# Performance work log

Measured on AMD Instinct MI355X. Metric: run time of the kernel, lower is better.

## Reference

```python
import jax, jax.numpy as jnp
import numpy as np

N_NODES = 100000
N_EDGES = 1600000
N_GRAPHS = 2000
N_FEAT = 13


def gcn_conv(x, edge_index, W, b, n):
    """PyG GCNConv: h = D^{-1/2}(A+I)D^{-1/2} X W + b (add_self_loops, symmetric norm)."""
    h = x @ W  # [n, out]
    loop = jnp.arange(n, dtype=edge_index.dtype)
    src = jnp.concatenate([edge_index[0], loop])  # message sources (x_j)
    dst = jnp.concatenate([edge_index[1], loop])  # aggregation targets
    deg = jax.ops.segment_sum(jnp.ones_like(dst, dtype=h.dtype), dst, num_segments=n)
    dinv = jnp.where(deg > 0, jax.lax.rsqrt(jnp.maximum(deg, 1e-12)), 0.0)
    norm = dinv[src] * dinv[dst]  # [E+n]
    out = jax.ops.segment_sum(h[src] * norm[:, None], dst, num_segments=n)
    return out + b


def setup_inputs() -> dict:
    key = jax.random.key(0)
    ks = jax.random.split(key, 12)
    d = {}
    d["x"] = jax.random.normal(ks[0], (N_NODES, N_FEAT), dtype=jnp.float32)
    d["edge_index"] = jax.random.randint(ks[1], (2, N_EDGES), 0, N_NODES, dtype=jnp.int32)
    d["batch"] = jnp.sort(jax.random.randint(ks[2], (N_NODES,), 0, N_GRAPHS, dtype=jnp.int32))
    def lin(k, i, o):
        return jax.random.normal(k, (i, o), dtype=jnp.float32) * (1.0 / np.sqrt(i))
    d["W0"] = lin(ks[3], N_FEAT, 128); d["b0"] = jnp.zeros((128,), jnp.float32)
    d["W1"] = lin(ks[4], 128, 128);    d["b1"] = jnp.zeros((128,), jnp.float32)
    d["W2"] = lin(ks[5], 128, 128);    d["b2"] = jnp.zeros((128,), jnp.float32)
    d["Wf0"] = lin(ks[6], 128, 256);   d["bf0"] = jnp.zeros((256,), jnp.float32)
    d["Wf1"] = lin(ks[7], 256, 128);   d["bf1"] = jnp.zeros((128,), jnp.float32)
    d["Wo"] = lin(ks[8], 128, 1);      d["bo"] = jnp.zeros((1,), jnp.float32)
    return d


def reference(x, edge_index, batch, W0, b0, W1, b1, W2, b2, Wf0, bf0, Wf1, bf1, Wo, bo):
    n = x.shape[0]
    h = jax.nn.relu(gcn_conv(x, edge_index, W0, b0, n))
    h = jax.nn.relu(gcn_conv(h, edge_index, W1, b1, n))
    h = gcn_conv(h, edge_index, W2, b2, n)  # no relu after last conv
    # global mean pool over graphs
    cnt = jax.ops.segment_sum(jnp.ones((n,), h.dtype), batch, num_segments=N_GRAPHS)
    pooled = jax.ops.segment_sum(h, batch, num_segments=N_GRAPHS) / jnp.maximum(cnt, 1.0)[:, None]
    h = jax.nn.relu(pooled @ Wf0 + bf0)
    h = jax.nn.relu(h @ Wf1 + bf1)
    return h @ Wo + bo  # [N_GRAPHS, 1]
```

## Files before the change

kernel.cpp:

```cpp
#include <hip/hip_runtime.h>
#include <hip/hip_bf16.h>

#define N_NODES  100000
#define N_EDGES  1600000
#define N_GRAPHS 2000
#define N_FEAT   13
#define HID      128
#define NB       ((N_NODES + 127) / 128)
#define NBLK     128
#define N2       (NB * NBLK)

typedef __attribute__((ext_vector_type(8))) short bf16x8;
typedef __attribute__((ext_vector_type(4))) float f32x4;
typedef __attribute__((ext_vector_type(8))) unsigned short ushort8;

__global__ void k_hist1(const int* __restrict__ dst, int* __restrict__ counts, int E) {
    __shared__ int hist[NB];
    int k = blockIdx.x, t = threadIdx.x;
    for (int b = t; b < NB; b += 256) hist[b] = 0;
    __syncthreads();
    int epb = (E + NBLK - 1) / NBLK;
    int base = k * epb, lim = min(base + epb, E);
    for (int i = base + t; i < lim; i += 256) atomicAdd(&hist[dst[i] >> 7], 1);
    __syncthreads();
    for (int b = t; b < NB; b += 256) counts[k * NB + b] = hist[b];
}

__global__ void k_transp(const int* __restrict__ counts, int* __restrict__ countsT) {
    int i = blockIdx.x * 256 + threadIdx.x;
    if (i < N2) countsT[i] = counts[(i & (NBLK - 1)) * NB + (i >> 7)];
}

__global__ void k_scatter(const int* __restrict__ src, const int* __restrict__ dst,
                          const int* __restrict__ scT, unsigned int* __restrict__ bstore, int E) {
    __shared__ int cnt[NB];
    int k = blockIdx.x, t = threadIdx.x;
    for (int b = t; b < NB; b += 256) cnt[b] = 0;
    __syncthreads();
    int epb = (E + NBLK - 1) / NBLK;
    int base = k * epb, lim = min(base + epb, E);
    for (int i = base + t; i < lim; i += 256) {
        int d = dst[i];
        int b = d >> 7;
        int r = atomicAdd(&cnt[b], 1);
        bstore[scT[b * NBLK + k] + r] = ((unsigned int)src[i] << 7) | (unsigned int)(d & 127);
    }
}

__global__ void k_bhistx(const unsigned int* __restrict__ bstore, const int* __restrict__ scT,
                         const float* __restrict__ x, int* __restrict__ indeg,
                         float* __restrict__ dinv, float* __restrict__ xs, int n, int E) {
    __shared__ int cnt[128];
    int b = blockIdx.x, t = threadIdx.x;
    if (t < 128) cnt[t] = 0;
    __syncthreads();
    int start = scT[b * NBLK];
    int end = (b + 1 < NB) ? scT[(b + 1) * NBLK] : E;
    for (int i = start + t; i < end; i += 256) atomicAdd(&cnt[bstore[i] & 127], 1);
    __syncthreads();
    int node = b * 128 + t;
    if (t < 128 && node < n) {
        int c = cnt[t];
        indeg[node] = c;
        float dv = rsqrtf((float)(c + 1));
        dinv[node] = dv;
        float r[16];
#pragma unroll
        for (int k = 0; k < N_FEAT; k++) r[k] = dv * x[node * N_FEAT + k];
        r[13] = r[14] = r[15] = 0.f;
        float4* o = (float4*)&xs[(size_t)node * 16];
        o[0] = float4{r[0], r[1], r[2], r[3]};
        o[1] = float4{r[4], r[5], r[6], r[7]};
        o[2] = float4{r[8], r[9], r[10], r[11]};
        o[3] = float4{r[12], r[13], r[14], r[15]};
    }
}

__global__ void k_bfill(const unsigned int* __restrict__ bstore, const int* __restrict__ scT,
                        const int* __restrict__ off, int* __restrict__ csr, int n, int E) {
    __shared__ int cur[128];
    __shared__ int loff[128];
    int b = blockIdx.x, t = threadIdx.x;
    if (t < 128) {
        cur[t] = 0;
        int node = b * 128 + t;
        loff[t] = (node < n) ? off[node] : 0;
    }
    __syncthreads();
    int start = scT[b * NBLK];
    int end = (b + 1 < NB) ? scT[(b + 1) * NBLK] : E;
    for (int i = start + t; i < end; i += 256) {
        unsigned int e = bstore[i];
        int dl = e & 127;
        int p = loff[dl] + atomicAdd(&cur[dl], 1);
        csr[p] = (int)(e >> 7);
    }
}

__global__ void k_scan1(const int* __restrict__ in, int* __restrict__ out,
                        int* __restrict__ bsum, int n) {
    __shared__ int ts[256];
    int t = threadIdx.x;
    int base = blockIdx.x * 1024 + t * 4;
    int v0 = (base + 0 < n) ? in[base + 0] : 0;
    int v1 = (base + 1 < n) ? in[base + 1] : 0;
    int v2 = (base + 2 < n) ? in[base + 2] : 0;
    int v3 = (base + 3 < n) ? in[base + 3] : 0;
    int s = v0 + v1 + v2 + v3;
    ts[t] = s;
    __syncthreads();
    for (int o = 1; o < 256; o <<= 1) {
        int x = (t >= o) ? ts[t - o] : 0;
        __syncthreads();
        ts[t] += x;
        __syncthreads();
    }
    if (t == 255) bsum[blockIdx.x] = ts[255];
    int run = ts[t] - s;
    if (base + 0 < n) out[base + 0] = run; run += v0;
    if (base + 1 < n) out[base + 1] = run; run += v1;
    if (base + 2 < n) out[base + 2] = run; run += v2;
    if (base + 3 < n) out[base + 3] = run;
}

__global__ void k_scan_block(const int* __restrict__ in, int* __restrict__ out, int len) {
    __shared__ int ts[256];
    int t = threadIdx.x;
    int v[8];
    int s = 0;
#pragma unroll
    for (int j = 0; j < 8; j++) {
        int i = t * 8 + j;
        v[j] = (i < len) ? in[i] : 0;
        s += v[j];
    }
    ts[t] = s;
    __syncthreads();
    for (int o = 1; o < 256; o <<= 1) {
        int x = (t >= o) ? ts[t - o] : 0;
        __syncthreads();
        ts[t] += x;
        __syncthreads();
    }
    int run = ts[t] - s;
#pragma unroll
    for (int j = 0; j < 8; j++) {
        int i = t * 8 + j;
        if (i < len) out[i] = run;
        run += v[j];
    }
}

__global__ void k_scan3(int* __restrict__ out, const int* __restrict__ bpre, int n) {
    int i = blockIdx.x * 256 + threadIdx.x;
    if (i < n) out[i] += bpre[i >> 10];
}

__device__ __forceinline__ unsigned short f2bf(float f) {
    unsigned int b = __float_as_uint(f);
    b += 0x7fffu + ((b >> 16) & 1u);
    return (unsigned short)(b >> 16);
}

__device__ __forceinline__ void addrow8(float (&a)[8], uint4 v) {
    a[0] += __uint_as_float(v.x << 16);
    a[1] += __uint_as_float(v.x & 0xffff0000u);
    a[2] += __uint_as_float(v.y << 16);
    a[3] += __uint_as_float(v.y & 0xffff0000u);
    a[4] += __uint_as_float(v.z << 16);
    a[5] += __uint_as_float(v.z & 0xffff0000u);
    a[6] += __uint_as_float(v.w << 16);
    a[7] += __uint_as_float(v.w & 0xffff0000u);
}

__global__ __launch_bounds__(256) void k_gf13(const float* __restrict__ xs,
                                              const int* __restrict__ off,
                                              const int* __restrict__ indeg,
                                              const int* __restrict__ csr,
                                              const float* __restrict__ dinv,
                                              const float* __restrict__ W,
                                              const float* __restrict__ b,
                                              unsigned short* __restrict__ h, int n) {
    __shared__ float Ws[N_FEAT * HID];
    __shared__ __align__(16) float aggs[64][16];
    __shared__ float bs[HID];
    int t = threadIdx.x;
    for (int i = t; i < N_FEAT * HID; i += 256) Ws[i] = W[i];
    if (t < HID) bs[t] = b[t];
    int lane = t & 63;
    int slot = (t >> 6) * 16 + (lane >> 2);
    int l2 = lane & 3;
    int nb = blockIdx.x * 64;
    int d = nb + slot;
    const float4* X4 = (const float4*)xs;
    if (d < n) {
        int s0 = off[d], c = indeg[d];
        float4 acc = X4[(size_t)d * 4 + l2];
        int p = 0;
        for (; p + 7 < c; p += 8) {
            int s_[8];
#pragma unroll
            for (int j = 0; j < 8; j++) s_[j] = csr[s0 + p + j];
            float4 v[8];
#pragma unroll
            for (int j = 0; j < 8; j++) v[j] = X4[(size_t)s_[j] * 4 + l2];
#pragma unroll
            for (int j = 0; j < 8; j++) {
                acc.x += v[j].x; acc.y += v[j].y; acc.z += v[j].z; acc.w += v[j].w;
            }
        }
        for (; p < c; p++) {
            float4 v = X4[(size_t)csr[s0 + p] * 4 + l2];
            acc.x += v.x; acc.y += v.y; acc.z += v.z; acc.w += v.w;
        }
        float dv = dinv[d];
        float4 r = {dv * acc.x, dv * acc.y, dv * acc.z, dv * acc.w};
        *(float4*)&aggs[slot][l2 * 4] = r;
    }
    __syncthreads();
    int f = t & 127;
    int g0 = t >> 7;
    float wreg[N_FEAT];
#pragma unroll
    for (int k = 0; k < N_FEAT; k++) wreg[k] = Ws[k * HID + f];
#pragma unroll
    for (int j = 0; j < 32; j++) {
        int nl = g0 + j * 2;
        int dd = nb + nl;
        if (dd < n) {
            float acc = bs[f];
#pragma unroll
            for (int k = 0; k < N_FEAT; k++) acc += aggs[nl][k] * wreg[k];
            h[(size_t)dd * HID + f] = f2bf(fmaxf(acc, 0.f));
        }
    }
}

__global__ void k_wcast2(const float* __restrict__ W1, const float* __restrict__ W2,
                         unsigned short* __restrict__ Wt1, unsigned short* __restrict__ Wt2) {
    int i = blockIdx.x * 256 + threadIdx.x;
    if (i < HID * HID) {
        int c = i >> 7, k = i & 127;
        Wt1[i] = f2bf(W1[k * HID + c]);
        Wt2[i] = f2bf(W2[k * HID + c]);
    }
}

__global__ __launch_bounds__(256) void k_mfma128(const unsigned short* __restrict__ X,
                                                 const unsigned short* __restrict__ Wt,
                                                 const float* __restrict__ dinv,
                                                 unsigned short* __restrict__ ubf, int n) {
    int t = threadIdx.x;
    int wave = t >> 6, lane = t & 63;
    int lrow = lane & 15;
    int lk8 = (lane >> 4) * 8;
    int tile0 = blockIdx.x * 16 + wave * 4;

    f32x4 acc[4][8];
#pragma unroll
    for (int nt = 0; nt < 4; nt++)
#pragma unroll
        for (int ct = 0; ct < 8; ct++) acc[nt][ct] = f32x4{0.f, 0.f, 0.f, 0.f};

#pragma unroll
    for (int s = 0; s < 4; s++) {
        bf16x8 bfr[8];
#pragma unroll
        for (int ct = 0; ct < 8; ct++) {
            int col = ct * 16 + lrow;
            bfr[ct] = *(const bf16x8*)&Wt[col * HID + s * 32 + lk8];
        }
#pragma unroll
        for (int nt = 0; nt < 4; nt++) {
            int row = min((tile0 + nt) * 16 + lrow, n - 1);
            bf16x8 afr = *(const bf16x8*)&X[(size_t)row * HID + s * 32 + lk8];
#pragma unroll
            for (int ct = 0; ct < 8; ct++)
                acc[nt][ct] = __builtin_amdgcn_mfma_f32_16x16x32_bf16(afr, bfr[ct], acc[nt][ct], 0, 0, 0);
        }
    }

#pragma unroll
    for (int nt = 0; nt < 4; nt++) {
        int rbase = (tile0 + nt) * 16 + (lane >> 4) * 4;
#pragma unroll
        for (int r = 0; r < 4; r++) {
            int row = rbase + r;
            if (row < n) {
                float dv = dinv[row];
#pragma unroll
                for (int ct = 0; ct < 8; ct++)
                    ubf[(size_t)row * HID + ct * 16 + lrow] = f2bf(dv * acc[nt][ct][r]);
            }
        }
    }
}

__global__ void k_gather128(const unsigned int* __restrict__ ubf, const int* __restrict__ off,
                            const int* __restrict__ indeg, const int* __restrict__ csr,
                            const float* __restrict__ dinv, const float* __restrict__ bias,
                            unsigned short* __restrict__ yh, int n) {
    int t = threadIdx.x;
    int lane = t & 63;
    int quad = lane >> 4, l4 = lane & 15;
    int d = blockIdx.x * 16 + (t >> 6) * 4 + quad;
    if (d >= n) return;
    int s0 = off[d], c = indeg[d];
    const uint4* U = (const uint4*)ubf;

    uint4 sv = U[(size_t)d * 16 + l4];
    float a[8] = {0.f, 0.f, 0.f, 0.f, 0.f, 0.f, 0.f, 0.f};
    addrow8(a, sv);

    int p = 0;
    for (; p + 7 < c; p += 8) {
        int s_[8];
#pragma unroll
        for (int j = 0; j < 8; j++) s_[j] = csr[s0 + p + j];
        uint4 v[8];
#pragma unroll
        for (int j = 0; j < 8; j++) v[j] = U[(size_t)s_[j] * 16 + l4];
#pragma unroll
        for (int j = 0; j < 8; j++) addrow8(a, v[j]);
    }
    if (p + 3 < c) {
        int s_[4];
#pragma unroll
        for (int j = 0; j < 4; j++) s_[j] = csr[s0 + p + j];
        uint4 v[4];
#pragma unroll
        for (int j = 0; j < 4; j++) v[j] = U[(size_t)s_[j] * 16 + l4];
#pragma unroll
        for (int j = 0; j < 4; j++) addrow8(a, v[j]);
        p += 4;
    }
    for (; p < c; p++) addrow8(a, U[(size_t)csr[s0 + p] * 16 + l4]);

    float dv = dinv[d];
    float4 bb0 = *(const float4*)&bias[l4 * 8];
    float4 bb1 = *(const float4*)&bias[l4 * 8 + 4];
    float r[8];
    r[0] = dv * a[0] + bb0.x; r[1] = dv * a[1] + bb0.y;
    r[2] = dv * a[2] + bb0.z; r[3] = dv * a[3] + bb0.w;
    r[4] = dv * a[4] + bb1.x; r[5] = dv * a[5] + bb1.y;
    r[6] = dv * a[6] + bb1.z; r[7] = dv * a[7] + bb1.w;
    ushort8 hh;
#pragma unroll
    for (int j = 0; j < 8; j++) hh[j] = f2bf(fmaxf(r[j], 0.f));
    *(ushort8*)&yh[(size_t)d * HID + l4 * 8] = hh;
}

__global__ void k_gather128p(const unsigned int* __restrict__ ubf, const int* __restrict__ off,
                             const int* __restrict__ indeg, const int* __restrict__ csr,
                             const float* __restrict__ dinv, const float* __restrict__ bias,
                             const int* __restrict__ batch, float* __restrict__ pooledm, int n) {
    __shared__ __align__(16) float part[16][128];
    __shared__ int bid[16];
    int t = threadIdx.x;
    int lane = t & 63;
    int quad = lane >> 4, l4 = lane & 15;
    int slot = (t >> 6) * 4 + quad;
    int d = blockIdx.x * 16 + slot;
    const uint4* U = (const uint4*)ubf;
    if (d < n) {
        int s0 = off[d], c = indeg[d];
        uint4 sv = U[(size_t)d * 16 + l4];
        float a[8] = {0.f, 0.f, 0.f, 0.f, 0.f, 0.f, 0.f, 0.f};
        addrow8(a, sv);
        int p = 0;
        for (; p + 7 < c; p += 8) {
            int s_[8];
#pragma unroll
            for (int j = 0; j < 8; j++) s_[j] = csr[s0 + p + j];
            uint4 v[8];
#pragma unroll
            for (int j = 0; j < 8; j++) v[j] = U[(size_t)s_[j] * 16 + l4];
#pragma unroll
            for (int j = 0; j < 8; j++) addrow8(a, v[j]);
        }
        if (p + 3 < c) {
            int s_[4];
#pragma unroll
            for (int j = 0; j < 4; j++) s_[j] = csr[s0 + p + j];
            uint4 v[4];
#pragma unroll
            for (int j = 0; j < 4; j++) v[j] = U[(size_t)s_[j] * 16 + l4];
#pragma unroll
            for (int j = 0; j < 4; j++) addrow8(a, v[j]);
            p += 4;
        }
        for (; p < c; p++) addrow8(a, U[(size_t)csr[s0 + p] * 16 + l4]);

        float dv = dinv[d];
        float4 bb0 = *(const float4*)&bias[l4 * 8];
        float4 bb1 = *(const float4*)&bias[l4 * 8 + 4];
        float4 r0 = {dv * a[0] + bb0.x, dv * a[1] + bb0.y, dv * a[2] + bb0.z, dv * a[3] + bb0.w};
        float4 r1 = {dv * a[4] + bb1.x, dv * a[5] + bb1.y, dv * a[6] + bb1.z, dv * a[7] + bb1.w};
        *(float4*)&part[slot][l4 * 8] = r0;
        *(float4*)&part[slot][l4 * 8 + 4] = r1;
        if (l4 == 0) bid[slot] = batch[d];
    } else {
        if (l4 == 0) bid[slot] = -1;
    }
    __syncthreads();
    if (t < 128) {
        int f = t;
        float acc = 0.f;
        int g = -1;
        for (int j = 0; j < 16; j++) {
            int bj = bid[j];
            if (bj < 0) break;
            if (bj != g) {
                if (g >= 0) atomicAdd(&pooledm[g * HID + f], acc);
                g = bj; acc = 0.f;
            }
            acc += part[j][f];
        }
        if (g >= 0) atomicAdd(&pooledm[g * HID + f], acc);
    }
}

__global__ void k_cnt(const int* __restrict__ batch, int* __restrict__ cnt, int n) {
    int i = blockIdx.x * 256 + threadIdx.x;
    if (i < n) atomicAdd(&cnt[batch[i]], 1);
}

__global__ void k_fc0(const float* __restrict__ in, const int* __restrict__ cnt,
                      const float* __restrict__ W, const float* __restrict__ b,
                      float* __restrict__ out) {
    __shared__ float row[128];
    int g = blockIdx.x, t = threadIdx.x;
    if (t < 128) row[t] = in[g * 128 + t] * (1.f / (float)max(cnt[g], 1));
    __syncthreads();
    float acc = 0.f;
#pragma unroll 8
    for (int k = 0; k < 128; k++) acc += row[k] * W[k * 256 + t];
    acc += b[t];
    out[g * 256 + t] = fmaxf(acc, 0.f);
}

__global__ void k_fc1(const float* __restrict__ in, const float* __restrict__ W,
                      const float* __restrict__ b, float* __restrict__ out) {
    __shared__ float row[256];
    int g = blockIdx.x, t = threadIdx.x;
    row[t] = in[g * 256 + t];
    row[t + 128] = in[g * 256 + t + 128];
    __syncthreads();
    float acc = 0.f;
#pragma unroll 8
    for (int k = 0; k < 256; k++) acc += row[k] * W[k * 128 + t];
    acc += b[t];
    out[g * 128 + t] = fmaxf(acc, 0.f);
}

__global__ void k_fco(const float* __restrict__ in, const float* __restrict__ Wo,
                      const float* __restrict__ bo, float* __restrict__ out) {
    int g = blockIdx.x, t = threadIdx.x;
    float acc = in[g * 128 + t] * Wo[t] + in[g * 128 + 64 + t] * Wo[64 + t];
    for (int s = 32; s > 0; s >>= 1) acc += __shfl_down(acc, s);
    if (t == 0) out[g] = acc + bo[0];
}

extern "C" void kernel_launch(void* const* d_in, const int* in_sizes, int n_in,
                              void* d_out, int out_size, void* d_ws, size_t ws_size,
                              hipStream_t stream) {
    const float* x   = (const float*)d_in[0];
    const int* ei    = (const int*)d_in[1];
    const int* src   = ei;
    const int* dst   = ei + N_EDGES;
    const int* batch = (const int*)d_in[2];
    const float* W0 = (const float*)d_in[3];  const float* b0 = (const float*)d_in[4];
    const float* W1 = (const float*)d_in[5];  const float* b1 = (const float*)d_in[6];
    const float* W2 = (const float*)d_in[7];  const float* b2 = (const float*)d_in[8];
    const float* Wf0 = (const float*)d_in[9];  const float* bf0 = (const float*)d_in[10];
    const float* Wf1 = (const float*)d_in[11]; const float* bf1 = (const float*)d_in[12];
    const float* Wo = (const float*)d_in[13];  const float* bo = (const float*)d_in[14];
    float* out = (float*)d_out;

    char* w = (char*)d_ws;
    size_t o = 0;
    auto take = [&](size_t bytes) -> char* {
        char* p = w + o;
        o += (bytes + 255) & ~(size_t)255;
        return p;
    };
    int* indeg    = (int*)take((size_t)N_NODES * 4);
    int* off      = (int*)take((size_t)N_NODES * 4);
    int* counts   = (int*)take((size_t)N2 * 4);
    int* countsT  = (int*)take((size_t)N2 * 4);
    int* scT      = (int*)take((size_t)N2 * 4);
    int* bsum     = (int*)take(256 * 4);
    int* bpre     = (int*)take(256 * 4);
    int* csr      = (int*)take((size_t)N_EDGES * 4);
    float* dinv   = (float*)take((size_t)N_NODES * 4);
    int* cnt      = (int*)take((size_t)N_GRAPHS * 4);
    float* xs     = (float*)take((size_t)N_NODES * 16 * 4);
    unsigned short* hbf0 = (unsigned short*)take((size_t)N_NODES * HID * 2);
    unsigned short* hbf1 = (unsigned short*)take((size_t)N_NODES * HID * 2);
    unsigned short* ubf  = (unsigned short*)take((size_t)N_NODES * HID * 2);
    unsigned short* Wt1  = (unsigned short*)take((size_t)HID * HID * 2);
    unsigned short* Wt2  = (unsigned short*)take((size_t)HID * HID * 2);
    float* pooledm= (float*)take((size_t)N_GRAPHS * HID * 4);
    float* fc0    = (float*)take((size_t)N_GRAPHS * 256 * 4);
    float* fc1    = (float*)take((size_t)N_GRAPHS * HID * 4);
    unsigned int* bstore = (unsigned int*)ubf;

    hipMemsetAsync(cnt, 0, (size_t)N_GRAPHS * 4, stream);
    hipMemsetAsync(pooledm, 0, (size_t)N_GRAPHS * HID * 4, stream);

    k_hist1<<<NBLK, 256, 0, stream>>>(dst, counts, N_EDGES);
    k_transp<<<(N2 + 255) / 256, 256, 0, stream>>>(counts, countsT);
    int nb2 = (N2 + 1023) / 1024;
    k_scan1<<<nb2, 256, 0, stream>>>(countsT, scT, bsum, N2);
    k_scan_block<<<1, 256, 0, stream>>>(bsum, bpre, nb2);
    k_scan3<<<(N2 + 255) / 256, 256, 0, stream>>>(scT, bpre, N2);
    k_scatter<<<NBLK, 256, 0, stream>>>(src, dst, scT, bstore, N_EDGES);
    k_bhistx<<<NB, 256, 0, stream>>>(bstore, scT, x, indeg, dinv, xs, N_NODES, N_EDGES);
    int nb1 = (N_NODES + 1023) / 1024;
    k_scan1<<<nb1, 256, 0, stream>>>(indeg, off, bsum, N_NODES);
    k_scan_block<<<1, 256, 0, stream>>>(bsum, bpre, nb1);
    k_scan3<<<(N_NODES + 255) / 256, 256, 0, stream>>>(off, bpre, N_NODES);
    k_bfill<<<NB, 256, 0, stream>>>(bstore, scT, off, csr, N_NODES, N_EDGES);
    k_cnt<<<(N_NODES + 255) / 256, 256, 0, stream>>>(batch, cnt, N_NODES);
    k_wcast2<<<(HID * HID + 255) / 256, 256, 0, stream>>>(W1, W2, Wt1, Wt2);

    k_gf13<<<(N_NODES + 63) / 64, 256, 0, stream>>>(xs, off, indeg, csr, dinv, W0, b0, hbf0, N_NODES);
    k_mfma128<<<(N_NODES + 255) / 256, 256, 0, stream>>>(hbf0, Wt1, dinv, ubf, N_NODES);
    k_gather128<<<(N_NODES + 15) / 16, 256, 0, stream>>>((const unsigned int*)ubf, off, indeg, csr, dinv, b1, hbf1, N_NODES);
    k_mfma128<<<(N_NODES + 255) / 256, 256, 0, stream>>>(hbf1, Wt2, dinv, ubf, N_NODES);
    k_gather128p<<<(N_NODES + 15) / 16, 256, 0, stream>>>((const unsigned int*)ubf, off, indeg, csr, dinv, b2, batch, pooledm, N_NODES);

    k_fc0<<<N_GRAPHS, 256, 0, stream>>>(pooledm, cnt, Wf0, bf0, fc0);
    k_fc1<<<N_GRAPHS, 128, 0, stream>>>(fc0, Wf1, bf1, fc1);
    k_fco<<<N_GRAPHS, 64, 0, stream>>>(fc1, Wo, bo, out);
}
```

Measured before the change: 350.4 us.

## Fuse CSR build scans and MLP head, double scatter blocks

Raises the number of edge-partition blocks for histogram and scatter from 128 to 256. The transpose kernel is folded into the first scan, which reads counts in transposed order. Node offsets are now computed by a per-bucket prefix scan inside k_bhistx, which removes the separate three-kernel node-degree scan. The three head kernels are merged into one so intermediates stay in shared memory. This cuts kernel launches and global round-trips, at the cost of a larger count matrix, strided reads in the scan, and a shared-memory row padded to 132 floats.

```diff
diff --git a/kernel.cpp b/kernel.cpp
--- a/kernel.cpp
+++ b/kernel.cpp
@@ -7,7 +7,8 @@
 #define N_FEAT   13
 #define HID      128
 #define NB       ((N_NODES + 127) / 128)
-#define NBLK     128
+#define NBLK     256
+#define LOG_NBLK 8
 #define N2       (NB * NBLK)
 
 typedef __attribute__((ext_vector_type(8))) short bf16x8;
@@ -26,9 +27,63 @@
     for (int b = t; b < NB; b += 256) counts[k * NB + b] = hist[b];
 }
 
-__global__ void k_transp(const int* __restrict__ counts, int* __restrict__ countsT) {
+__global__ void k_scan1T(const int* __restrict__ counts, int* __restrict__ out,
+                         int* __restrict__ bsum, int n2) {
+    __shared__ int ts[256];
+    int t = threadIdx.x;
+    int base = blockIdx.x * 1024 + t * 4;
+    auto ld = [&](int i) -> int {
+        return (i < n2) ? counts[(i & (NBLK - 1)) * NB + (i >> LOG_NBLK)] : 0;
+    };
+    int v0 = ld(base + 0), v1 = ld(base + 1), v2 = ld(base + 2), v3 = ld(base + 3);
+    int s = v0 + v1 + v2 + v3;
+    ts[t] = s;
+    __syncthreads();
+    for (int o = 1; o < 256; o <<= 1) {
+        int x = (t >= o) ? ts[t - o] : 0;
+        __syncthreads();
+        ts[t] += x;
+        __syncthreads();
+    }
+    if (t == 255) bsum[blockIdx.x] = ts[255];
+    int run = ts[t] - s;
+    if (base + 0 < n2) out[base + 0] = run; run += v0;
+    if (base + 1 < n2) out[base + 1] = run; run += v1;
+    if (base + 2 < n2) out[base + 2] = run; run += v2;
+    if (base + 3 < n2) out[base + 3] = run;
+}
+
+__global__ void k_scan_block(const int* __restrict__ in, int* __restrict__ out, int len) {
+    __shared__ int ts[256];
+    int t = threadIdx.x;
+    int v[8];
+    int s = 0;
+#pragma unroll
+    for (int j = 0; j < 8; j++) {
+        int i = t * 8 + j;
+        v[j] = (i < len) ? in[i] : 0;
+        s += v[j];
+    }
+    ts[t] = s;
+    __syncthreads();
+    for (int o = 1; o < 256; o <<= 1) {
+        int x = (t >= o) ? ts[t - o] : 0;
+        __syncthreads();
+        ts[t] += x;
+        __syncthreads();
+    }
+    int run = ts[t] - s;
+#pragma unroll
+    for (int j = 0; j < 8; j++) {
+        int i = t * 8 + j;
+        if (i < len) out[i] = run;
+        run += v[j];
+    }
+}
+
+__global__ void k_scan3(int* __restrict__ out, const int* __restrict__ bpre, int n) {
     int i = blockIdx.x * 256 + threadIdx.x;
-    if (i < N2) countsT[i] = counts[(i & (NBLK - 1)) * NB + (i >> 7)];
+    if (i < n) out[i] += bpre[i >> 10];
 }
 
 __global__ void k_scatter(const int* __restrict__ src, const int* __restrict__ dst,
@@ -49,8 +104,10 @@
 
 __global__ void k_bhistx(const unsigned int* __restrict__ bstore, const int* __restrict__ scT,
                          const float* __restrict__ x, int* __restrict__ indeg,
-                         float* __restrict__ dinv, float* __restrict__ xs, int n, int E) {
+                         float* __restrict__ dinv, float* __restrict__ xs,
+                         int* __restrict__ off, int n, int E) {
     __shared__ int cnt[128];
+    __shared__ int pre[128];
     int b = blockIdx.x, t = threadIdx.x;
     if (t < 128) cnt[t] = 0;
     __syncthreads();
@@ -58,21 +115,30 @@
     int end = (b + 1 < NB) ? scT[(b + 1) * NBLK] : E;
     for (int i = start + t; i < end; i += 256) atomicAdd(&cnt[bstore[i] & 127], 1);
     __syncthreads();
+    if (t < 128) pre[t] = cnt[t];
+    __syncthreads();
+    for (int o = 1; o < 128; o <<= 1) {
+        int v = (t < 128 && t >= o) ? pre[t - o] : 0;
+        __syncthreads();
+        if (t < 128) pre[t] += v;
+        __syncthreads();
+    }
     int node = b * 128 + t;
     if (t < 128 && node < n) {
         int c = cnt[t];
         indeg[node] = c;
+        off[node] = start + pre[t] - c;
         float dv = rsqrtf((float)(c + 1));
         dinv[node] = dv;
         float r[16];
 #pragma unroll
         for (int k = 0; k < N_FEAT; k++) r[k] = dv * x[node * N_FEAT + k];
         r[13] = r[14] = r[15] = 0.f;
-        float4* o = (float4*)&xs[(size_t)node * 16];
-        o[0] = float4{r[0], r[1], r[2], r[3]};
-        o[1] = float4{r[4], r[5], r[6], r[7]};
-        o[2] = float4{r[8], r[9], r[10], r[11]};
-        o[3] = float4{r[12], r[13], r[14], r[15]};
+        float4* o4 = (float4*)&xs[(size_t)node * 16];
+        o4[0] = float4{r[0], r[1], r[2], r[3]};
+        o4[1] = float4{r[4], r[5], r[6], r[7]};
+        o4[2] = float4{r[8], r[9], r[10], r[11]};
+        o4[3] = float4{r[12], r[13], r[14], r[15]};
     }
 }
 
@@ -95,65 +161,6 @@
         int p = loff[dl] + atomicAdd(&cur[dl], 1);
         csr[p] = (int)(e >> 7);
     }
-}
-
-__global__ void k_scan1(const int* __restrict__ in, int* __restrict__ out,
-                        int* __restrict__ bsum, int n) {
-    __shared__ int ts[256];
-    int t = threadIdx.x;
-    int base = blockIdx.x * 1024 + t * 4;
-    int v0 = (base + 0 < n) ? in[base + 0] : 0;
-    int v1 = (base + 1 < n) ? in[base + 1] : 0;
-    int v2 = (base + 2 < n) ? in[base + 2] : 0;
-    int v3 = (base + 3 < n) ? in[base + 3] : 0;
-    int s = v0 + v1 + v2 + v3;
-    ts[t] = s;
-    __syncthreads();
-    for (int o = 1; o < 256; o <<= 1) {
-        int x = (t >= o) ? ts[t - o] : 0;
-        __syncthreads();
-        ts[t] += x;
-        __syncthreads();
-    }
-    if (t == 255) bsum[blockIdx.x] = ts[255];
-    int run = ts[t] - s;
-    if (base + 0 < n) out[base + 0] = run; run += v0;
-    if (base + 1 < n) out[base + 1] = run; run += v1;
-    if (base + 2 < n) out[base + 2] = run; run += v2;
-    if (base + 3 < n) out[base + 3] = run;
-}
-
-__global__ void k_scan_block(const int* __restrict__ in, int* __restrict__ out, int len) {
-    __shared__ int ts[256];
-    int t = threadIdx.x;
-    int v[8];
-    int s = 0;
-#pragma unroll
-    for (int j = 0; j < 8; j++) {
-        int i = t * 8 + j;
-        v[j] = (i < len) ? in[i] : 0;
-        s += v[j];
-    }
-    ts[t] = s;
-    __syncthreads();
-    for (int o = 1; o < 256; o <<= 1) {
-        int x = (t >= o) ? ts[t - o] : 0;
-        __syncthreads();
-        ts[t] += x;
-        __syncthreads();
-    }
-    int run = ts[t] - s;
-#pragma unroll
-    for (int j = 0; j < 8; j++) {
-        int i = t * 8 + j;
-        if (i < len) out[i] = run;
-        run += v[j];
-    }
-}
-
-__global__ void k_scan3(int* __restrict__ out, const int* __restrict__ bpre, int n) {
-    int i = blockIdx.x * 256 + threadIdx.x;
-    if (i < n) out[i] += bpre[i >> 10];
 }
 
 __device__ __forceinline__ unsigned short f2bf(float f) {
@@ -354,7 +361,7 @@
                              const int* __restrict__ indeg, const int* __restrict__ csr,
                              const float* __restrict__ dinv, const float* __restrict__ bias,
                              const int* __restrict__ batch, float* __restrict__ pooledm, int n) {
-    __shared__ __align__(16) float part[16][128];
+    __shared__ __align__(16) float part[16][132];
     __shared__ int bid[16];
     int t = threadIdx.x;
     int lane = t & 63;
@@ -364,9 +371,8 @@
     const uint4* U = (const uint4*)ubf;
     if (d < n) {
         int s0 = off[d], c = indeg[d];
-        uint4 sv = U[(size_t)d * 16 + l4];
         float a[8] = {0.f, 0.f, 0.f, 0.f, 0.f, 0.f, 0.f, 0.f};
-        addrow8(a, sv);
+        addrow8(a, U[(size_t)d * 16 + l4]);
         int p = 0;
         for (; p + 7 < c; p += 8) {
             int s_[8];
@@ -425,40 +431,36 @@
     if (i < n) atomicAdd(&cnt[batch[i]], 1);
 }
 
-__global__ void k_fc0(const float* __restrict__ in, const int* __restrict__ cnt,
-                      const float* __restrict__ W, const float* __restrict__ b,
-                      float* __restrict__ out) {
+__global__ void k_head(const float* __restrict__ pooledm, const int* __restrict__ cnt,
+                       const float* __restrict__ Wf0, const float* __restrict__ bf0,
+                       const float* __restrict__ Wf1, const float* __restrict__ bf1,
+                       const float* __restrict__ Wo, const float* __restrict__ bo,
+                       float* __restrict__ out) {
     __shared__ float row[128];
+    __shared__ float f0[256];
+    __shared__ float f1[128];
     int g = blockIdx.x, t = threadIdx.x;
-    if (t < 128) row[t] = in[g * 128 + t] * (1.f / (float)max(cnt[g], 1));
-    __syncthreads();
-    float acc = 0.f;
+    if (t < 128) row[t] = pooledm[g * 128 + t] * (1.f / (float)max(cnt[g], 1));
+    __syncthreads();
+    {
+        float acc = 0.f;
 #pragma unroll 8
-    for (int k = 0; k < 128; k++) acc += row[k] * W[k * 256 + t];
-    acc += b[t];
-    out[g * 256 + t] = fmaxf(acc, 0.f);
-}
-
-__global__ void k_fc1(const float* __restrict__ in, const float* __restrict__ W,
-                      const float* __restrict__ b, float* __restrict__ out) {
-    __shared__ float row[256];
-    int g = blockIdx.x, t = threadIdx.x;
-    row[t] = in[g * 256 + t];
-    row[t + 128] = in[g * 256 + t + 128];
-    __syncthreads();
-    float acc = 0.f;
+        for (int k = 0; k < 128; k++) acc += row[k] * Wf0[k * 256 + t];
+        f0[t] = fmaxf(acc + bf0[t], 0.f);
+    }
+    __syncthreads();
+    if (t < 128) {
+        float acc = 0.f;
 #pragma unroll 8
-    for (int k = 0; k < 256; k++) acc += row[k] * W[k * 128 + t];
-    acc += b[t];
-    out[g * 128 + t] = fmaxf(acc, 0.f);
-}
-
-__global__ void k_fco(const float* __restrict__ in, const float* __restrict__ Wo,
-                      const float* __restrict__ bo, float* __restrict__ out) {
-    int g = blockIdx.x, t = threadIdx.x;
-    float acc = in[g * 128 + t] * Wo[t] + in[g * 128 + 64 + t] * Wo[64 + t];
-    for (int s = 32; s > 0; s >>= 1) acc += __shfl_down(acc, s);
-    if (t == 0) out[g] = acc + bo[0];
+        for (int k = 0; k < 256; k++) acc += f0[k] * Wf1[k * 128 + t];
+        f1[t] = fmaxf(acc + bf1[t], 0.f);
+    }
+    __syncthreads();
+    if (t < 64) {
+        float acc = f1[t] * Wo[t] + f1[t + 64] * Wo[64 + t];
+        for (int s = 32; s > 0; s >>= 1) acc += __shfl_down(acc, s);
+        if (t == 0) out[g] = acc + bo[0];
+    }
 }
 
 extern "C" void kernel_launch(void* const* d_in, const int* in_sizes, int n_in,
@@ -487,7 +489,6 @@
     int* indeg    = (int*)take((size_t)N_NODES * 4);
     int* off      = (int*)take((size_t)N_NODES * 4);
     int* counts   = (int*)take((size_t)N2 * 4);
-    int* countsT  = (int*)take((size_t)N2 * 4);
     int* scT      = (int*)take((size_t)N2 * 4);
     int* bsum     = (int*)take(256 * 4);
     int* bpre     = (int*)take(256 * 4);
@@ -501,25 +502,18 @@
     unsigned short* Wt1  = (unsigned short*)take((size_t)HID * HID * 2);
     unsigned short* Wt2  = (unsigned short*)take((size_t)HID * HID * 2);
     float* pooledm= (float*)take((size_t)N_GRAPHS * HID * 4);
-    float* fc0    = (float*)take((size_t)N_GRAPHS * 256 * 4);
-    float* fc1    = (float*)take((size_t)N_GRAPHS * HID * 4);
     unsigned int* bstore = (unsigned int*)ubf;
 
     hipMemsetAsync(cnt, 0, (size_t)N_GRAPHS * 4, stream);
     hipMemsetAsync(pooledm, 0, (size_t)N_GRAPHS * HID * 4, stream);
 
     k_hist1<<<NBLK, 256, 0, stream>>>(dst, counts, N_EDGES);
-    k_transp<<<(N2 + 255) / 256, 256, 0, stream>>>(counts, countsT);
     int nb2 = (N2 + 1023) / 1024;
-    k_scan1<<<nb2, 256, 0, stream>>>(countsT, scT, bsum, N2);
+    k_scan1T<<<nb2, 256, 0, stream>>>(counts, scT, bsum, N2);
     k_scan_block<<<1, 256, 0, stream>>>(bsum, bpre, nb2);
     k_scan3<<<(N2 + 255) / 256, 256, 0, stream>>>(scT, bpre, N2);
     k_scatter<<<NBLK, 256, 0, stream>>>(src, dst, scT, bstore, N_EDGES);
-    k_bhistx<<<NB, 256, 0, stream>>>(bstore, scT, x, indeg, dinv, xs, N_NODES, N_EDGES);
-    int nb1 = (N_NODES + 1023) / 1024;
-    k_scan1<<<nb1, 256, 0, stream>>>(indeg, off, bsum, N_NODES);
-    k_scan_block<<<1, 256, 0, stream>>>(bsum, bpre, nb1);
-    k_scan3<<<(N_NODES + 255) / 256, 256, 0, stream>>>(off, bpre, N_NODES);
+    k_bhistx<<<NB, 256, 0, stream>>>(bstore, scT, x, indeg, dinv, xs, off, N_NODES, N_EDGES);
     k_bfill<<<NB, 256, 0, stream>>>(bstore, scT, off, csr, N_NODES, N_EDGES);
     k_cnt<<<(N_NODES + 255) / 256, 256, 0, stream>>>(batch, cnt, N_NODES);
     k_wcast2<<<(HID * HID + 255) / 256, 256, 0, stream>>>(W1, W2, Wt1, Wt2);
@@ -530,7 +524,5 @@
     k_mfma128<<<(N_NODES + 255) / 256, 256, 0, stream>>>(hbf1, Wt2, dinv, ubf, N_NODES);
     k_gather128p<<<(N_NODES + 15) / 16, 256, 0, stream>>>((const unsigned int*)ubf, off, indeg, csr, dinv, b2, batch, pooledm, N_NODES);
 
-    k_fc0<<<N_GRAPHS, 256, 0, stream>>>(pooledm, cnt, Wf0, bf0, fc0);
-    k_fc1<<<N_GRAPHS, 128, 0, stream>>>(fc0, Wf1, bf1, fc1);
-    k_fco<<<N_GRAPHS, 64, 0, stream>>>(fc1, Wo, bo, out);
-}
+    k_head<<<N_GRAPHS, 256, 0, stream>>>(pooledm, cnt, Wf0, bf0, Wf1, bf1, Wo, bo, out);
+}
```

Measured after the change: 320.9 us. 1.09x faster.
